# Optimization experiments

Hardware: AMD Instinct MI355X
Metric: run time of the kernel (lower is better)

The kernel has to match this reference:

```python
import jax, jax.numpy as jnp
import numpy as np

N_NODES = 100000
N_PAIRS = 500000
DIM = 256


def setup_inputs() -> dict:
    key = jax.random.key(0)
    k1, k2, k3, k4, k5 = jax.random.split(key, 5)
    return {
        "p_vertices": jax.random.randint(k1, (N_PAIRS,), 0, N_NODES, dtype=jnp.int64) if jax.config.jax_enable_x64 else jax.random.randint(k1, (N_PAIRS,), 0, N_NODES).astype(jnp.int32),
        "q_vertices": jax.random.randint(k2, (N_PAIRS,), 0, N_NODES).astype(jnp.int32),
        "embedding": jax.random.normal(k3, (N_NODES, DIM), dtype=jnp.float32),
        "W1": jax.random.normal(k4, (DIM, DIM), dtype=jnp.float32) * (1.0 / np.sqrt(DIM)),
        "b1": jnp.zeros((DIM,), dtype=jnp.float32),
        "W2": jax.random.normal(k5, (DIM, 1), dtype=jnp.float32) * (1.0 / np.sqrt(DIM)),
        "b2": jnp.zeros((1,), dtype=jnp.float32),
    }


def reference(p_vertices, q_vertices, embedding, W1, b1, W2, b2):
    # gather rows for each pair: [M, 256]
    embd_i = embedding[p_vertices]
    embd_j = embedding[q_vertices]
    d = (embd_i - embd_j) ** 2            # squared difference, [M, 256]
    h = jax.nn.relu(d @ W1 + b1)          # MLP hidden, [M, 256]
    pred = h @ W2 + b2                    # [M, 1]
    return pred.squeeze(-1)               # [M]
```

## Files before the change

### kernel.cpp

```cpp
#include <hip/hip_runtime.h>
#include <hip/hip_bf16.h>

typedef __attribute__((ext_vector_type(8))) short s16x8;
typedef __attribute__((ext_vector_type(4))) float f32x4;
typedef _Float16 h16x8 __attribute__((ext_vector_type(8)));
typedef __fp16 fp16x2 __attribute__((ext_vector_type(2)));

__global__ void prep_w1t(const float* __restrict__ W1, short* __restrict__ W1T) {
    int t = blockIdx.x * 256 + threadIdx.x;
    int n = t >> 8, k = t & 255;
    union { _Float16 h; short s; } u;
    u.h = (_Float16)W1[k * 256 + n];
    W1T[t] = u.s;
}

__global__ void prep_emb16(const float* __restrict__ src, _Float16* __restrict__ dst,
                           int n8) {
    int t = blockIdx.x * 256 + threadIdx.x;
    if (t >= n8) return;
    const float4 a = ((const float4*)src)[t * 2];
    const float4 b = ((const float4*)src)[t * 2 + 1];
    h16x8 h;
    h[0] = (_Float16)a.x; h[1] = (_Float16)a.y;
    h[2] = (_Float16)a.z; h[3] = (_Float16)a.w;
    h[4] = (_Float16)b.x; h[5] = (_Float16)b.y;
    h[6] = (_Float16)b.z; h[7] = (_Float16)b.w;
    *(h16x8*)(dst + t * 8) = h;
}

#define NBLK 256

__global__ __launch_bounds__(1024)
void pair_mlp_f16(const int* __restrict__ pidx, const int* __restrict__ qidx,
                  const _Float16* __restrict__ emb, const short* __restrict__ w1t,
                  const float* __restrict__ b1, const float* __restrict__ w2,
                  const float* __restrict__ b2p, float* __restrict__ out,
                  int M, int NT)
{
    __shared__ short Blds[256 * 256];
    __shared__ short Abuf[2][128 * 64];
    float* Red = (float*)&Abuf[1][0];

    const int tid  = threadIdx.x;
    const int lane = tid & 63;
    const int wv   = tid >> 6;
    const int c    = lane & 15;
    const int g    = lane >> 4;
    const int cg   = wv & 7;
    const int rh   = wv >> 3;

#pragma unroll
    for (int it = 0; it < 8; ++it) {
        int G = it * 1024 + tid;
        int col = G >> 5, kg = G & 31;
        s16x8 v = *(const s16x8*)(w1t + G * 8);
        *(s16x8*)(Blds + (col * 32 + (kg ^ (col & 7))) * 8) = v;
    }

    f32x4 b1q[2];
    float w2v[2][4];
#pragma unroll
    for (int n = 0; n < 2; ++n)
#pragma unroll
        for (int j = 0; j < 4; ++j) {
            b1q[n][j]  = b1[cg * 32 + n * 16 + g * 4 + j];
            w2v[n][j]  = w2[cg * 32 + n * 16 + g * 4 + j];
        }
    const float b2v = b2p[0];
    __syncthreads();

    const int r  = tid >> 3;
    const int sg = tid & 7;
    const int wslot = (sg ^ (r & 7)) * 8;

    int im0 = blockIdx.x * 128 + r; im0 = im0 < M ? im0 : M - 1;
    int pi = pidx[im0], qi = qidx[im0];

    h16x8 wp[4], wq[4];

#define LD(W, PP, QP, S)                                                 \
    {                                                                    \
        wp[W] = *(const h16x8*)((PP) + (S) * 64);                        \
        wq[W] = *(const h16x8*)((QP) + (S) * 64);                        \
    }

#define CONV(W, BUF)                                                     \
    {                                                                    \
        h16x8 d = wp[W] - wq[W];                                         \
        h16x8 s = d * d;                                                 \
        *(h16x8*)(&Abuf[BUF][0] + r * 64 + wslot) = s;                   \
    }

#define MFMA_STEP(S, BUF)                                                \
    {                                                                    \
        const short* ab = &Abuf[BUF][0];                                 \
        __builtin_amdgcn_s_setprio(1);                                   \
        _Pragma("unroll")                                                \
        for (int kk = 0; kk < 2; ++kk) {                                 \
            int bs = ((S) * 8 + kk * 4 + g) ^ (c & 7);                   \
            h16x8 bf0 = *(const h16x8*)(Blds + ((cg * 32 + c) * 32 + bs) * 8);      \
            h16x8 bf1 = *(const h16x8*)(Blds + ((cg * 32 + 16 + c) * 32 + bs) * 8); \
            _Pragma("unroll")                                            \
            for (int m = 0; m < 4; ++m) {                                \
                int row = rh * 64 + m * 16 + c;                          \
                h16x8 af = *(const h16x8*)(ab + row * 64 +               \
                                           (((kk * 4 + g) ^ (c & 7)) * 8)); \
                acc[m][0] = __builtin_amdgcn_mfma_f32_16x16x32_f16(      \
                    bf0, af, acc[m][0], 0, 0, 0);                        \
                acc[m][1] = __builtin_amdgcn_mfma_f32_16x16x32_f16(      \
                    bf1, af, acc[m][1], 0, 0, 0);                        \
            }                                                            \
        }                                                                \
        __builtin_amdgcn_s_setprio(0);                                   \
    }

    {
        const _Float16* pp = emb + (size_t)pi * 256 + sg * 8;
        const _Float16* qp = emb + (size_t)qi * 256 + sg * 8;
        LD(0, pp, qp, 0)
        LD(1, pp, qp, 1)
        LD(2, pp, qp, 2)
    }

    for (int tile = blockIdx.x; tile < NT; tile += NBLK) {
        const int base = tile * 128;
        const _Float16* pp = emb + (size_t)pi * 256 + sg * 8;
        const _Float16* qp = emb + (size_t)qi * 256 + sg * 8;

        int pi_n = pi, qi_n = qi;
        {
            int t2 = tile + NBLK;
            if (t2 < NT) {
                int im2 = t2 * 128 + r; im2 = im2 < M ? im2 : M - 1;
                pi_n = pidx[im2]; qi_n = qidx[im2];
            }
        }

        CONV(0, 0)

        f32x4 acc[4][2];
#pragma unroll
        for (int m = 0; m < 4; ++m) { acc[m][0] = b1q[0]; acc[m][1] = b1q[1]; }

        __syncthreads();
        LD(3, pp, qp, 3)
        MFMA_STEP(0, 0)
        CONV(1, 1)

        const _Float16* pp_n = emb + (size_t)pi_n * 256 + sg * 8;
        const _Float16* qp_n = emb + (size_t)qi_n * 256 + sg * 8;

        __syncthreads();
        LD(0, pp_n, qp_n, 0)
        MFMA_STEP(1, 1)
        CONV(2, 0)
        __syncthreads();
        LD(1, pp_n, qp_n, 1)
        MFMA_STEP(2, 0)
        CONV(3, 1)
        __syncthreads();
        LD(2, pp_n, qp_n, 2)
        MFMA_STEP(3, 1)

        float part[4];
#pragma unroll
        for (int m = 0; m < 4; ++m) {
            float s = 0.f;
#pragma unroll
            for (int n = 0; n < 2; ++n)
#pragma unroll
                for (int j = 0; j < 4; ++j) {
                    float h = acc[m][n][j];
                    h = h > 0.f ? h : 0.f;
                    s += h * w2v[n][j];
                }
            part[m] = s;
        }
#pragma unroll
        for (int m = 0; m < 4; ++m) {
            part[m] += __shfl_xor(part[m], 16, 64);
            part[m] += __shfl_xor(part[m], 32, 64);
        }

        __syncthreads();
        if (g == 0) {
#pragma unroll
            for (int m = 0; m < 4; ++m)
                Red[cg * 128 + rh * 64 + m * 16 + c] = part[m];
        }
        __syncthreads();
        if (tid < 128) {
            int row = base + tid;
            if (row < M) {
                float s = b2v;
#pragma unroll
                for (int k = 0; k < 8; ++k) s += Red[k * 128 + tid];
                out[row] = s;
            }
        }
        pi = pi_n; qi = qi_n;
    }
#undef LD
#undef CONV
#undef MFMA_STEP
}

__global__ __launch_bounds__(1024)
void pair_mlp_f32(const int* __restrict__ pidx, const int* __restrict__ qidx,
                  const float* __restrict__ emb, const short* __restrict__ w1t,
                  const float* __restrict__ b1, const float* __restrict__ w2,
                  const float* __restrict__ b2p, float* __restrict__ out,
                  int M, int NT)
{
    __shared__ short Blds[256 * 256];
    __shared__ short Abuf[2][128 * 64];
    float* Red = (float*)&Abuf[1][0];

    const int tid  = threadIdx.x;
    const int lane = tid & 63;
    const int wv   = tid >> 6;
    const int c    = lane & 15;
    const int g    = lane >> 4;
    const int cg   = wv & 7;
    const int rh   = wv >> 3;

#pragma unroll
    for (int it = 0; it < 8; ++it) {
        int G = it * 1024 + tid;
        int col = G >> 5, kg = G & 31;
        s16x8 v = *(const s16x8*)(w1t + G * 8);
        *(s16x8*)(Blds + (col * 32 + (kg ^ (col & 7))) * 8) = v;
    }

    f32x4 b1q[2];
    float w2v[2][4];
#pragma unroll
    for (int n = 0; n < 2; ++n)
#pragma unroll
        for (int j = 0; j < 4; ++j) {
            b1q[n][j] = b1[cg * 32 + n * 16 + g * 4 + j];
            w2v[n][j] = w2[cg * 32 + n * 16 + g * 4 + j];
        }
    const float b2v = b2p[0];
    __syncthreads();

    const int r  = tid >> 3;
    const int sg = tid & 7;
    const int wslot = (sg ^ (r & 7)) * 8;

    int im0 = blockIdx.x * 128 + r; im0 = im0 < M ? im0 : M - 1;
    int pi = pidx[im0], qi = qidx[im0];

#define LOADW(W, S)                                                      \
    {                                                                    \
        const float* ps = pp + (S) * 64;                                 \
        const float* qs = qp + (S) * 64;                                 \
        P0_##W = ((const float4*)ps)[0]; P1_##W = ((const float4*)ps)[1];\
        Q0_##W = ((const float4*)qs)[0]; Q1_##W = ((const float4*)qs)[1];\
    }

#define CONVF(W, BUF)                                                    \
    {                                                                    \
        float d0 = P0_##W.x - Q0_##W.x, d1 = P0_##W.y - Q0_##W.y;        \
        float d2 = P0_##W.z - Q0_##W.z, d3 = P0_##W.w - Q0_##W.w;        \
        float d4 = P1_##W.x - Q1_##W.x, d5 = P1_##W.y - Q1_##W.y;        \
        float d6 = P1_##W.z - Q1_##W.z, d7 = P1_##W.w - Q1_##W.w;        \
        union { h16x8 v; fp16x2 p[4]; } a;                               \
        a.p[0] = __builtin_amdgcn_cvt_pkrtz(d0 * d0, d1 * d1);           \
        a.p[1] = __builtin_amdgcn_cvt_pkrtz(d2 * d2, d3 * d3);           \
        a.p[2] = __builtin_amdgcn_cvt_pkrtz(d4 * d4, d5 * d5);           \
        a.p[3] = __builtin_amdgcn_cvt_pkrtz(d6 * d6, d7 * d7);           \
        *(h16x8*)(&Abuf[BUF][0] + r * 64 + wslot) = a.v;                 \
    }

#define MFMA_STEPF(S, BUF)                                               \
    {                                                                    \
        const short* ab = &Abuf[BUF][0];                                 \
        _Pragma("unroll")                                                \
        for (int kk = 0; kk < 2; ++kk) {                                 \
            int bs = ((S) * 8 + kk * 4 + g) ^ (c & 7);                   \
            h16x8 bf0 = *(const h16x8*)(Blds + ((cg * 32 + c) * 32 + bs) * 8);      \
            h16x8 bf1 = *(const h16x8*)(Blds + ((cg * 32 + 16 + c) * 32 + bs) * 8); \
            _Pragma("unroll")                                            \
            for (int m = 0; m < 4; ++m) {                                \
                int row = rh * 64 + m * 16 + c;                          \
                h16x8 af = *(const h16x8*)(ab + row * 64 +               \
                                           (((kk * 4 + g) ^ (c & 7)) * 8)); \
                acc[m][0] = __builtin_amdgcn_mfma_f32_16x16x32_f16(      \
                    bf0, af, acc[m][0], 0, 0, 0);                        \
                acc[m][1] = __builtin_amdgcn_mfma_f32_16x16x32_f16(      \
                    bf1, af, acc[m][1], 0, 0, 0);                        \
            }                                                            \
        }                                                                \
    }

    for (int tile = blockIdx.x; tile < NT; tile += NBLK) {
        const int base = tile * 128;
        const float* pp = emb + (size_t)pi * 256 + sg * 8;
        const float* qp = emb + (size_t)qi * 256 + sg * 8;

        float4 P0_0, P1_0, Q0_0, Q1_0, P0_1, P1_1, Q0_1, Q1_1;
        LOADW(0, 0)
        LOADW(1, 1)

        int pi_n = pi, qi_n = qi;
        {
            int t2 = tile + NBLK;
            if (t2 < NT) {
                int im2 = t2 * 128 + r; im2 = im2 < M ? im2 : M - 1;
                pi_n = pidx[im2]; qi_n = qidx[im2];
            }
        }

        CONVF(0, 0)

        f32x4 acc[4][2];
#pragma unroll
        for (int m = 0; m < 4; ++m) { acc[m][0] = b1q[0]; acc[m][1] = b1q[1]; }

        __syncthreads();
        LOADW(0, 2)
        MFMA_STEPF(0, 0)
        CONVF(1, 1)
        __syncthreads();
        LOADW(1, 3)
        MFMA_STEPF(1, 1)
        CONVF(0, 0)
        __syncthreads();
        MFMA_STEPF(2, 0)
        CONVF(1, 1)
        __syncthreads();
        MFMA_STEPF(3, 1)

        float part[4];
#pragma unroll
        for (int m = 0; m < 4; ++m) {
            float s = 0.f;
#pragma unroll
            for (int n = 0; n < 2; ++n)
#pragma unroll
                for (int j = 0; j < 4; ++j) {
                    float h = acc[m][n][j];
                    h = h > 0.f ? h : 0.f;
                    s += h * w2v[n][j];
                }
            part[m] = s;
        }
#pragma unroll
        for (int m = 0; m < 4; ++m) {
            part[m] += __shfl_xor(part[m], 16, 64);
            part[m] += __shfl_xor(part[m], 32, 64);
        }

        __syncthreads();
        if (g == 0) {
#pragma unroll
            for (int m = 0; m < 4; ++m)
                Red[cg * 128 + rh * 64 + m * 16 + c] = part[m];
        }
        __syncthreads();
        if (tid < 128) {
            int row = base + tid;
            if (row < M) {
                float s = b2v;
#pragma unroll
                for (int k = 0; k < 8; ++k) s += Red[k * 128 + tid];
                out[row] = s;
            }
        }
        pi = pi_n; qi = qi_n;
    }
#undef LOADW
#undef CONVF
#undef MFMA_STEPF
}

extern "C" void kernel_launch(void* const* d_in, const int* in_sizes, int n_in,
                              void* d_out, int out_size, void* d_ws, size_t ws_size,
                              hipStream_t stream) {
    const int*   p   = (const int*)d_in[0];
    const int*   q   = (const int*)d_in[1];
    const float* emb = (const float*)d_in[2];
    const float* W1  = (const float*)d_in[3];
    const float* b1  = (const float*)d_in[4];
    const float* W2  = (const float*)d_in[5];
    const float* b2  = (const float*)d_in[6];
    float* out = (float*)d_out;
    int M = in_sizes[0];
    int embElems = in_sizes[2];
    int NT = (M + 127) / 128;

    short* w1t = (short*)d_ws;
    size_t embOff = 131072;
    size_t need = embOff + (size_t)embElems * 2;

    prep_w1t<<<256, 256, 0, stream>>>(W1, w1t);

    if (ws_size >= need) {
        _Float16* emb16 = (_Float16*)((char*)d_ws + embOff);
        int n8 = embElems / 8;
        prep_emb16<<<(n8 + 255) / 256, 256, 0, stream>>>(emb, emb16, n8);
        pair_mlp_f16<<<NBLK, 1024, 0, stream>>>(p, q, emb16, w1t, b1, W2, b2,
                                                out, M, NT);
    } else {
        pair_mlp_f32<<<NBLK, 1024, 0, stream>>>(p, q, emb, w1t, b1, W2, b2,
                                                out, M, NT);
    }
}
```

Measured before the change: 108.9 us.

## Retile f16 pair MLP to 192-row tiles with 768 threads and 8 K-slices

Result: slower. 128.4 us (+17.8%).

```diff
diff --git a/kernel.cpp b/kernel.cpp
--- a/kernel.cpp
+++ b/kernel.cpp
@@ -29,8 +29,9 @@
 }
 
 #define NBLK 256
-
-__global__ __launch_bounds__(1024)
+#define BM 192
+
+__global__ __launch_bounds__(768)
 void pair_mlp_f16(const int* __restrict__ pidx, const int* __restrict__ qidx,
                   const _Float16* __restrict__ emb, const short* __restrict__ w1t,
                   const float* __restrict__ b1, const float* __restrict__ w2,
@@ -38,7 +39,7 @@
                   int M, int NT)
 {
     __shared__ short Blds[256 * 256];
-    __shared__ short Abuf[2][128 * 64];
+    __shared__ short Abuf[2][BM * 32];
     float* Red = (float*)&Abuf[1][0];
 
     const int tid  = threadIdx.x;
@@ -46,84 +47,87 @@
     const int wv   = tid >> 6;
     const int c    = lane & 15;
     const int g    = lane >> 4;
-    const int cg   = wv & 7;
-    const int rh   = wv >> 3;
-
-#pragma unroll
-    for (int it = 0; it < 8; ++it) {
-        int G = it * 1024 + tid;
-        int col = G >> 5, kg = G & 31;
-        s16x8 v = *(const s16x8*)(w1t + G * 8);
-        *(s16x8*)(Blds + (col * 32 + (kg ^ (col & 7))) * 8) = v;
-    }
-
-    f32x4 b1q[2];
-    float w2v[2][4];
-#pragma unroll
-    for (int n = 0; n < 2; ++n)
-#pragma unroll
-        for (int j = 0; j < 4; ++j) {
-            b1q[n][j]  = b1[cg * 32 + n * 16 + g * 4 + j];
-            w2v[n][j]  = w2[cg * 32 + n * 16 + g * 4 + j];
-        }
+    const int wr   = wv >> 2;
+    const int wc   = wv & 3;
+
+#pragma unroll
+    for (int it = 0; it < 11; ++it) {
+        int G = it * 768 + tid;
+        if (G < 8192) {
+            int col = G >> 5, kg = G & 31;
+            s16x8 v = *(const s16x8*)(w1t + G * 8);
+            *(s16x8*)(Blds + (col * 32 + (kg ^ (col & 7))) * 8) = v;
+        }
+    }
+
     const float b2v = b2p[0];
+
+    int araddr[4];
+#pragma unroll
+    for (int m = 0; m < 4; ++m) {
+        int R = wr * 64 + m * 16 + c;
+        araddr[m] = R * 32 + ((g ^ ((R >> 1) & 3)) * 8);
+    }
+    int bcol[4];
+#pragma unroll
+    for (int n = 0; n < 4; ++n) bcol[n] = (wc * 64 + n * 16 + c) * 256;
+    const int bx = c & 7;
+
+    const int r  = tid >> 2;
+    const int sg = tid & 3;
+    const int wbase = r * 32 + ((sg ^ ((r >> 1) & 3)) * 8);
+
     __syncthreads();
 
-    const int r  = tid >> 3;
-    const int sg = tid & 7;
-    const int wslot = (sg ^ (r & 7)) * 8;
-
-    int im0 = blockIdx.x * 128 + r; im0 = im0 < M ? im0 : M - 1;
+    int im0 = blockIdx.x * BM + r; im0 = im0 < M ? im0 : M - 1;
     int pi = pidx[im0], qi = qidx[im0];
 
-    h16x8 wp[4], wq[4];
-
-#define LD(W, PP, QP, S)                                                 \
+    h16x8 wp0, wq0, wp1, wq1;
+
+#define LD(WP, WQ, PP, QP, S)                                            \
+    { WP = *(const h16x8*)((PP) + (S) * 32);                             \
+      WQ = *(const h16x8*)((QP) + (S) * 32); }
+
+#define CONV(WP, WQ, BUFI)                                               \
+    { h16x8 d = WP - WQ; h16x8 sq = d * d;                               \
+      *(h16x8*)(&Abuf[BUFI][0] + wbase) = sq; }
+
+#define MFMA_SLICE(S, BUFI)                                              \
     {                                                                    \
-        wp[W] = *(const h16x8*)((PP) + (S) * 64);                        \
-        wq[W] = *(const h16x8*)((QP) + (S) * 64);                        \
-    }
-
-#define CONV(W, BUF)                                                     \
-    {                                                                    \
-        h16x8 d = wp[W] - wq[W];                                         \
-        h16x8 s = d * d;                                                 \
-        *(h16x8*)(&Abuf[BUF][0] + r * 64 + wslot) = s;                   \
-    }
-
-#define MFMA_STEP(S, BUF)                                                \
-    {                                                                    \
-        const short* ab = &Abuf[BUF][0];                                 \
+        const short* ab = &Abuf[BUFI][0];                                \
+        h16x8 af0 = *(const h16x8*)(ab + araddr[0]);                     \
+        h16x8 af1 = *(const h16x8*)(ab + araddr[1]);                     \
+        h16x8 af2 = *(const h16x8*)(ab + araddr[2]);                     \
+        h16x8 af3 = *(const h16x8*)(ab + araddr[3]);                     \
         __builtin_amdgcn_s_setprio(1);                                   \
         _Pragma("unroll")                                                \
-        for (int kk = 0; kk < 2; ++kk) {                                 \
-            int bs = ((S) * 8 + kk * 4 + g) ^ (c & 7);                   \
-            h16x8 bf0 = *(const h16x8*)(Blds + ((cg * 32 + c) * 32 + bs) * 8);      \
-            h16x8 bf1 = *(const h16x8*)(Blds + ((cg * 32 + 16 + c) * 32 + bs) * 8); \
-            _Pragma("unroll")                                            \
-            for (int m = 0; m < 4; ++m) {                                \
-                int row = rh * 64 + m * 16 + c;                          \
-                h16x8 af = *(const h16x8*)(ab + row * 64 +               \
-                                           (((kk * 4 + g) ^ (c & 7)) * 8)); \
-                acc[m][0] = __builtin_amdgcn_mfma_f32_16x16x32_f16(      \
-                    bf0, af, acc[m][0], 0, 0, 0);                        \
-                acc[m][1] = __builtin_amdgcn_mfma_f32_16x16x32_f16(      \
-                    bf1, af, acc[m][1], 0, 0, 0);                        \
-            }                                                            \
+        for (int n = 0; n < 4; ++n) {                                    \
+            h16x8 bf = *(const h16x8*)(Blds + bcol[n] +                  \
+                                       ((((S) * 4 + g) ^ bx) * 8));      \
+            acc[0][n] = __builtin_amdgcn_mfma_f32_16x16x32_f16(bf, af0, acc[0][n], 0, 0, 0); \
+            acc[1][n] = __builtin_amdgcn_mfma_f32_16x16x32_f16(bf, af1, acc[1][n], 0, 0, 0); \
+            acc[2][n] = __builtin_amdgcn_mfma_f32_16x16x32_f16(bf, af2, acc[2][n], 0, 0, 0); \
+            acc[3][n] = __builtin_amdgcn_mfma_f32_16x16x32_f16(bf, af3, acc[3][n], 0, 0, 0); \
         }                                                                \
         __builtin_amdgcn_s_setprio(0);                                   \
     }
+
+#define SLICE(S, WPa, WQa, WPb, WQb, PPs, QPs, SS)                       \
+    __syncthreads();                                                     \
+    LD(WPa, WQa, PPs, QPs, SS)                                           \
+    MFMA_SLICE(S, (S) & 1)                                               \
+    CONV(WPb, WQb, ((S) + 1) & 1)
 
     {
         const _Float16* pp = emb + (size_t)pi * 256 + sg * 8;
         const _Float16* qp = emb + (size_t)qi * 256 + sg * 8;
-        LD(0, pp, qp, 0)
-        LD(1, pp, qp, 1)
-        LD(2, pp, qp, 2)
+        LD(wp0, wq0, pp, qp, 0)
+        LD(wp1, wq1, pp, qp, 1)
+        CONV(wp0, wq0, 0)
     }
 
     for (int tile = blockIdx.x; tile < NT; tile += NBLK) {
-        const int base = tile * 128;
+        const int base = tile * BM;
         const _Float16* pp = emb + (size_t)pi * 256 + sg * 8;
         const _Float16* qp = emb + (size_t)qi * 256 + sg * 8;
 
@@ -131,50 +135,53 @@
         {
             int t2 = tile + NBLK;
             if (t2 < NT) {
-                int im2 = t2 * 128 + r; im2 = im2 < M ? im2 : M - 1;
+                int im2 = t2 * BM + r; im2 = im2 < M ? im2 : M - 1;
                 pi_n = pidx[im2]; qi_n = qidx[im2];
             }
         }
-
-        CONV(0, 0)
-
-        f32x4 acc[4][2];
-#pragma unroll
-        for (int m = 0; m < 4; ++m) { acc[m][0] = b1q[0]; acc[m][1] = b1q[1]; }
-
-        __syncthreads();
-        LD(3, pp, qp, 3)
-        MFMA_STEP(0, 0)
-        CONV(1, 1)
-
         const _Float16* pp_n = emb + (size_t)pi_n * 256 + sg * 8;
         const _Float16* qp_n = emb + (size_t)qi_n * 256 + sg * 8;
 
-        __syncthreads();
-        LD(0, pp_n, qp_n, 0)
-        MFMA_STEP(1, 1)
-        CONV(2, 0)
-        __syncthreads();
-        LD(1, pp_n, qp_n, 1)
-        MFMA_STEP(2, 0)
-        CONV(3, 1)
-        __syncthreads();
-        LD(2, pp_n, qp_n, 2)
-        MFMA_STEP(3, 1)
+        f32x4 acc[4][4];
+        {
+            f32x4 b1q[4];
+#pragma unroll
+            for (int n = 0; n < 4; ++n)
+                b1q[n] = *(const f32x4*)(b1 + wc * 64 + n * 16 + g * 4);
+#pragma unroll
+            for (int m = 0; m < 4; ++m)
+#pragma unroll
+                for (int n = 0; n < 4; ++n) acc[m][n] = b1q[n];
+        }
+
+        SLICE(0, wp0, wq0, wp1, wq1, pp, qp, 2)
+        SLICE(1, wp1, wq1, wp0, wq0, pp, qp, 3)
+        SLICE(2, wp0, wq0, wp1, wq1, pp, qp, 4)
+        SLICE(3, wp1, wq1, wp0, wq0, pp, qp, 5)
+        SLICE(4, wp0, wq0, wp1, wq1, pp, qp, 6)
+        SLICE(5, wp1, wq1, wp0, wq0, pp, qp, 7)
+        SLICE(6, wp0, wq0, wp1, wq1, pp_n, qp_n, 0)
+        SLICE(7, wp1, wq1, wp0, wq0, pp_n, qp_n, 1)
 
         float part[4];
-#pragma unroll
-        for (int m = 0; m < 4; ++m) {
-            float s = 0.f;
-#pragma unroll
-            for (int n = 0; n < 2; ++n)
-#pragma unroll
-                for (int j = 0; j < 4; ++j) {
-                    float h = acc[m][n][j];
-                    h = h > 0.f ? h : 0.f;
-                    s += h * w2v[n][j];
-                }
-            part[m] = s;
+        {
+            f32x4 w2q[4];
+#pragma unroll
+            for (int n = 0; n < 4; ++n)
+                w2q[n] = *(const f32x4*)(w2 + wc * 64 + n * 16 + g * 4);
+#pragma unroll
+            for (int m = 0; m < 4; ++m) {
+                float s = 0.f;
+#pragma unroll
+                for (int n = 0; n < 4; ++n)
+#pragma unroll
+                    for (int j = 0; j < 4; ++j) {
+                        float h = acc[m][n][j];
+                        h = h > 0.f ? h : 0.f;
+                        s += h * w2q[n][j];
+                    }
+                part[m] = s;
+            }
         }
 #pragma unroll
         for (int m = 0; m < 4; ++m) {
@@ -186,23 +193,21 @@
         if (g == 0) {
 #pragma unroll
             for (int m = 0; m < 4; ++m)
-                Red[cg * 128 + rh * 64 + m * 16 + c] = part[m];
-        }
-        __syncthreads();
-        if (tid < 128) {
+                Red[wc * BM + wr * 64 + m * 16 + c] = part[m];
+        }
+        __syncthreads();
+        if (tid < BM) {
             int row = base + tid;
-            if (row < M) {
-                float s = b2v;
-#pragma unroll
-                for (int k = 0; k < 8; ++k) s += Red[k * 128 + tid];
-                out[row] = s;
-            }
+            if (row < M)
+                out[row] = b2v + Red[tid] + Red[BM + tid] +
+                           Red[2 * BM + tid] + Red[3 * BM + tid];
         }
         pi = pi_n; qi = qi_n;
     }
 #undef LD
 #undef CONV
-#undef MFMA_STEP
+#undef MFMA_SLICE
+#undef SLICE
 }
 
 __global__ __launch_bounds__(1024)
@@ -388,7 +393,7 @@
     float* out = (float*)d_out;
     int M = in_sizes[0];
     int embElems = in_sizes[2];
-    int NT = (M + 127) / 128;
+    int NT = (M + BM - 1) / BM;
 
     short* w1t = (short*)d_ws;
     size_t embOff = 131072;
@@ -400,10 +405,11 @@
         _Float16* emb16 = (_Float16*)((char*)d_ws + embOff);
         int n8 = embElems / 8;
         prep_emb16<<<(n8 + 255) / 256, 256, 0, stream>>>(emb, emb16, n8);
-        pair_mlp_f16<<<NBLK, 1024, 0, stream>>>(p, q, emb16, w1t, b1, W2, b2,
-                                                out, M, NT);
+        pair_mlp_f16<<<NBLK, 768, 0, stream>>>(p, q, emb16, w1t, b1, W2, b2,
+                                               out, M, NT);
     } else {
+        int NT128 = (M + 127) / 128;
         pair_mlp_f32<<<NBLK, 1024, 0, stream>>>(p, q, emb, w1t, b1, W2, b2,
-                                                out, M, NT);
+                                                out, M, NT128);
     }
 }
```
